# Performance work log

Measured on AMD Instinct MI355X. Metric: run time of the kernel, lower is better.

## Reference

```python
import jax, jax.numpy as jnp
import numpy as np

N_WAY = 5
K_SHOT = 5
TEMPERATURE = 1.0
NEG = -1e9  # emulates 'column does not exist' for pad columns beyond umask_length
EPS = 1e-12  # matches torch F.normalize eps


def _l2n(x, axis):
    n = jnp.sqrt(jnp.sum(x * x, axis=axis, keepdims=True))
    return x / jnp.maximum(n, EPS)


def setup_inputs() -> dict:
    key = jax.random.key(0)
    k1, k2, k3, k4, k5 = jax.random.split(key, 5)
    b, c, h, w = 4, 64, 5, 5
    q, u = 75, 100
    support_xf = jax.random.normal(k1, (b, N_WAY * K_SHOT, c, h, w), jnp.float32)
    query_xf = jax.random.normal(k2, (b, q, c, h, w), jnp.float32)
    unlabeled_xf = jax.random.normal(k3, (b, u, c, h, w), jnp.float32)
    support_y = jax.random.randint(k4, (b, N_WAY * K_SHOT), 0, N_WAY)
    query_y = jax.random.randint(k5, (b, q), 0, N_WAY)
    return {"support_xf": support_xf, "support_y": support_y, "query_xf": query_xf,
            "query_y": query_y, "unlabeled_xf": unlabeled_xf}


def _forward(support_xf, query_xf, unlabeled_xf, query_y):
    b, q, c, h, w = query_xf.shape
    M_s = K_SHOT * h * w
    unl = unlabeled_xf.reshape(b, -1, c, h, w)
    u = unl.shape[1]
    M_u = u * h * w
    # pooled unlabeled local descriptors, flattened in (u, h, w) order -> [b, c, M_u]
    unl_feat = unl.transpose(0, 2, 1, 3, 4).reshape(b, c, M_u)
    # support -> [b, n_way, c, k_shot*h*w]
    sup = support_xf.reshape(b, N_WAY, K_SHOT, c, h, w).transpose(0, 1, 3, 2, 4, 5).reshape(b, N_WAY, c, M_s)
    # cosine similarity unlabeled -> support: [b, n_way, M_u, M_s]
    u2s = jnp.einsum('bwcn,bcm->bwmn', _l2n(sup, 2), _l2n(unl_feat, 1))
    pool = u2s.transpose(0, 2, 1, 3).reshape(b, M_u, N_WAY * M_s)
    s_nearest = jnp.argmax(pool, axis=1)          # per support loc: nearest unlabeled loc
    u_nearest = jnp.argmax(pool, axis=2)          # per unlabeled loc: nearest support loc
    mutual = jnp.take_along_axis(s_nearest, u_nearest, axis=1) == jnp.arange(M_u)[None, :]  # [b, M_u]
    # class with max similarity per unlabeled location
    cls = jnp.argmax(jnp.max(u2s, axis=-1), axis=1)  # [b, M_u]
    umask = jax.nn.one_hot(cls, N_WAY, dtype=jnp.float32).transpose(0, 2, 1) \
            * mutual[:, None, :].astype(jnp.float32)  # [b, n_way, M_u]
    counts = umask.sum(-1)                          # [b, n_way]
    L = counts.max()                                # umask_length (traced)
    # stream compaction via stable argsort of the 0/1 mask (preserves original order)
    order = jnp.argsort(-umask, axis=-1)            # jnp.argsort is stable
    pts = unl_feat.transpose(0, 2, 1)               # [b, M_u, c]
    gath = jnp.take_along_axis(pts[:, None, :, :], order[..., None], axis=2)  # [b, n_way, M_u, c]
    valid = (jnp.arange(M_u)[None, None, :] < counts[:, :, None]).astype(jnp.float32)
    comp = gath * valid[..., None]                  # rows beyond count are zeros (as in torch)
    s_cat = jnp.concatenate([sup, comp.transpose(0, 1, 3, 2)], axis=-1)  # [b, n_way, c, M_s+M_u]
    M_tot = M_s + M_u
    qn = _l2n(query_xf.reshape(b, q, c, h * w), 2)
    scn = _l2n(s_cat, 2)
    sim = jnp.einsum('bqcm,bwcn->bqwmn', qn, scn)   # [b, q, n_way, M_q, M_tot]
    sim = (sim + 1.0) * 0.5                          # FourLayer_64F branch
    # columns beyond umask_length don't exist in the torch dense tensor -> exclude from maxes
    pad = jnp.arange(M_tot)[None, None, None, None, :] >= (M_s + L)
    sim = jnp.where(pad, NEG, sim)
    M_q = h * w
    qm = sim.transpose(0, 1, 3, 2, 4).reshape(b, q, M_q, N_WAY * M_tot)
    support_nearest = jnp.argmax(qm, axis=2)        # [b, q, n_way*M_tot]
    query_nearest = jnp.argmax(qm, axis=3)          # [b, q, M_q]
    g = jnp.take_along_axis(support_nearest, query_nearest, axis=2)
    q_mask = (g == jnp.arange(M_q)[None, None, :]).astype(sim.dtype)  # mutual NN mask
    query_value = (jnp.max(sim, axis=-1) * q_mask[:, :, None, :]).sum(-1)  # [b, q, n_way]
    logits = query_value.reshape(b * q, N_WAY) / TEMPERATURE
    y = query_y.reshape(b * q)
    logp = jax.nn.log_softmax(logits, axis=-1)
    loss = -jnp.take_along_axis(logp, y[:, None], axis=1).mean()
    return loss


def reference(support_xf, support_y, query_xf, query_y, unlabeled_xf):
    return _forward(support_xf, query_xf, unlabeled_xf, query_y)
```

## Files before the change

### kernel.cpp

```cpp
#include <hip/hip_runtime.h>

#define NEGINF (-1e30f)

constexpr size_t OF_UNL  = 0;
constexpr size_t OF_COLT = OF_UNL  + (size_t)4*2500*64;
constexpr size_t OF_QT   = OF_COLT + (size_t)20*64*256;
constexpr size_t OF_ROWV = OF_QT   + (size_t)300*64*25;
constexpr size_t OF_ROWI = OF_ROWV + (size_t)4*5*8*2500;
constexpr size_t OF_CVI  = OF_ROWI + (size_t)4*5*8*2500;
constexpr size_t OF_CMP  = OF_CVI  + (size_t)4*5*125*20*2;
constexpr size_t OF_CNT  = OF_CMP  + (size_t)4*5*2500;
constexpr size_t OF_UNEAR= OF_CNT  + 20;
constexpr size_t OF_SNEAR= OF_UNEAR+ 10000;
constexpr size_t OF_BV   = OF_SNEAR+ 2500;
constexpr size_t OF_BP   = OF_BV   + 37500;
constexpr size_t OF_AMX  = OF_BP   + 37500;

__global__ __launch_bounds__(256) void knorm(
    const float* __restrict__ sup, const float* __restrict__ qry,
    const float* __restrict__ unl,
    float* __restrict__ unl_n, float* __restrict__ colT,
    float* __restrict__ qt)
{
    int gid = blockIdx.x * 256 + threadIdx.x;
    int loc = gid >> 4;
    int sub = gid & 15;
    if (loc >= 20000) return;

    const float* src;
    float* dst1; int dstr1;

    if (loc < 10000) {
        int b = loc / 2500, m = loc % 2500;
        int u = m / 25, hw = m % 25;
        src  = unl + ((size_t)(b*100 + u) * 64) * 25 + hw;
        dst1 = unl_n + (size_t)loc * 64; dstr1 = 1;
    } else if (loc < 12500) {
        int idx = loc - 10000;
        int b = idx / 625, r = idx % 625;
        int w = r / 125,  n = r % 125;
        int shot = n / 25, hw = n % 25;
        src  = sup + ((size_t)(b*25 + w*5 + shot) * 64) * 25 + hw;
        dst1 = colT + ((size_t)(b*5 + w) * 64) * 256 + n; dstr1 = 256;
    } else {
        int idx = loc - 12500;
        int bq = idx / 25, mq = idx % 25;
        src  = qry + ((size_t)bq * 64) * 25 + mq;
        dst1 = qt + ((size_t)bq * 25 + mq) * 64; dstr1 = 1;
    }

    float v[4]; float ss = 0.f;
    int c0 = sub * 4;
#pragma unroll
    for (int j = 0; j < 4; ++j) { v[j] = src[(size_t)(c0 + j) * 25]; ss += v[j] * v[j]; }
#pragma unroll
    for (int msk = 1; msk < 16; msk <<= 1) ss += __shfl_xor(ss, msk);
    float sc = 1.f / fmaxf(sqrtf(ss), 1e-12f);
#pragma unroll
    for (int j = 0; j < 4; ++j)
        dst1[(size_t)(c0 + j) * dstr1] = v[j] * sc;
}

__global__ __launch_bounds__(256) void kb(
    const float* __restrict__ unl_n, const float* __restrict__ colT,
    float* __restrict__ rowv, int* __restrict__ rowi, float* __restrict__ colvi)
{
    int bid = blockIdx.x;
    int nc = bid & 3;
    int mb = (bid >> 2) % 20;
    int bw = bid / 80;
    int b  = bw / 5;
    int tid = threadIdx.x;
    int lane = tid & 63, wv = tid >> 6;

    __shared__ float uls[128 * 65];
    __shared__ float sls[64 * 36];
    __shared__ float sv_[4][32];
    __shared__ int   si_[4][32];

    int m0 = mb * 128;
    int n0 = nc * 32;

    for (int i = tid; i < 128 * 16; i += 256) {
        int row = i >> 4, c4 = (i & 15) * 4;
        int m = m0 + row;
        float4 x = make_float4(0.f, 0.f, 0.f, 0.f);
        if (m < 2500) x = *(const float4*)(unl_n + ((size_t)(b * 2500 + m)) * 64 + c4);
        uls[row * 65 + c4 + 0] = x.x;
        uls[row * 65 + c4 + 1] = x.y;
        uls[row * 65 + c4 + 2] = x.z;
        uls[row * 65 + c4 + 3] = x.w;
    }
    {
        int c = tid >> 2, q = tid & 3;
        const float* sp = colT + ((size_t)bw * 64 + c) * 256 + n0 + q * 8;
        float4 a = *(const float4*)sp;
        float4 d4 = *(const float4*)(sp + 4);
        float* d = &sls[c * 36 + q * 8];
        d[0] = a.x; d[1] = a.y; d[2] = a.z; d[3] = a.w;
        d[4] = d4.x; d[5] = d4.y; d[6] = d4.z; d[7] = d4.w;
    }
    __syncthreads();

    int ml = tid & 127;
    int m  = m0 + ml;
    int nh = tid >> 7;
    int nbase = nh * 16;
    int nn_total = (125 - n0) < 32 ? (125 - n0) : 32;
    const float* myrow = &uls[ml * 65];

    float acc[16];
#pragma unroll
    for (int j = 0; j < 16; ++j) acc[j] = 0.f;

    for (int c = 0; c < 64; ++c) {
        float uv = myrow[c];
        const float4* sr = (const float4*)&sls[c * 36 + nbase];
        float4 s0 = sr[0], s1 = sr[1], s2 = sr[2], s3 = sr[3];
        acc[0]  = fmaf(uv, s0.x, acc[0]);  acc[1]  = fmaf(uv, s0.y, acc[1]);
        acc[2]  = fmaf(uv, s0.z, acc[2]);  acc[3]  = fmaf(uv, s0.w, acc[3]);
        acc[4]  = fmaf(uv, s1.x, acc[4]);  acc[5]  = fmaf(uv, s1.y, acc[5]);
        acc[6]  = fmaf(uv, s1.z, acc[6]);  acc[7]  = fmaf(uv, s1.w, acc[7]);
        acc[8]  = fmaf(uv, s2.x, acc[8]);  acc[9]  = fmaf(uv, s2.y, acc[9]);
        acc[10] = fmaf(uv, s2.z, acc[10]); acc[11] = fmaf(uv, s2.w, acc[11]);
        acc[12] = fmaf(uv, s3.x, acc[12]); acc[13] = fmaf(uv, s3.y, acc[13]);
        acc[14] = fmaf(uv, s3.z, acc[14]); acc[15] = fmaf(uv, s3.w, acc[15]);
    }

    int nnloc = nn_total - nbase;
    nnloc = nnloc < 0 ? 0 : (nnloc > 16 ? 16 : nnloc);
    float rbv = NEGINF; int rbi = 0;
    for (int j = 0; j < nnloc; ++j)
        if (acc[j] > rbv) { rbv = acc[j]; rbi = n0 + nbase + j; }
    if (m < 2500) {
        int ck = nc * 2 + nh;
        rowv[((size_t)bw * 8 + ck) * 2500 + m] = rbv;
        rowi[((size_t)bw * 8 + ck) * 2500 + m] = rbi;
    }

#pragma unroll
    for (int j = 0; j < 16; ++j) {
        float v = (m < 2500 && (nbase + j) < nn_total) ? acc[j] : NEGINF;
        float vm = v;
#pragma unroll
        for (int s2 = 1; s2 < 64; s2 <<= 1) vm = fmaxf(vm, __shfl_xor(vm, s2));
        unsigned long long msk = __ballot(v == vm);
        int first = __ffsll((unsigned long long)msk) - 1;
        if (lane == 0) { sv_[wv][nbase + j] = vm; si_[wv][nbase + j] = m0 + (wv & 1) * 64 + first; }
    }
    __syncthreads();
    if (tid < nn_total) {
        int w0 = (tid < 16) ? 0 : 2;
        float v = sv_[w0][tid];     int vi = si_[w0][tid];
        float v2 = sv_[w0 + 1][tid]; int i2 = si_[w0 + 1][tid];
        if (v2 > v || (v2 == v && i2 < vi)) { v = v2; vi = i2; }
        float* cv = colvi + ((((size_t)bw) * 125 + (n0 + tid)) * 20 + mb) * 2;
        cv[0] = v; ((int*)cv)[1] = vi;
    }
}

__global__ __launch_bounds__(256) void kmerge(
    const float* __restrict__ rowv, const int* __restrict__ rowi,
    const float* __restrict__ colvi,
    int* __restrict__ unear, int* __restrict__ snear)
{
    int it = blockIdx.x * 256 + threadIdx.x;
    if (it < 10000) {
        int b = it / 2500, m = it % 2500;
        float bv = NEGINF; int bi = 0;
#pragma unroll
        for (int w = 0; w < 5; ++w) {
#pragma unroll
            for (int ck = 0; ck < 8; ++ck) {
                size_t o = (((size_t)(b * 5 + w)) * 8 + ck) * 2500 + m;
                float v = rowv[o];
                if (v > bv) { bv = v; bi = w * 125 + rowi[o]; }
            }
        }
        unear[it] = bi;
    } else if (it < 12500) {
        int idx = it - 10000;
        const float* p = colvi + (size_t)idx * 40;
        float bv = NEGINF; int bi = 0x7fffffff;
        for (int mb2 = 0; mb2 < 20; ++mb2) {
            float v = p[mb2 * 2]; int vi = ((const int*)p)[mb2 * 2 + 1];
            if (v > bv || (v == bv && vi < bi)) { bv = v; bi = vi; }
        }
        snear[idx] = bi;
    }
}

__global__ __launch_bounds__(256) void kcmp(
    const int* __restrict__ unear, const int* __restrict__ snear,
    const float* __restrict__ unl_n,
    int* __restrict__ cmp, int* __restrict__ cntg, float* __restrict__ colT)
{
    int p = blockIdx.x;
    int b = p / 5, way = p % 5;
    int tid = threadIdx.x, lane = tid & 63, wv = tid >> 6;
    __shared__ unsigned long long masks[40];
    __shared__ int base[40];
    __shared__ int tot_s;

    for (int ch = wv; ch < 40; ch += 4) {
        int m = ch * 64 + lane;
        bool ok = false;
        if (m < 2500) {
            int un = unear[b * 2500 + m];
            ok = (un / 125 == way) && (snear[b * 625 + un] == m);
        }
        unsigned long long msk = __ballot(ok ? 1 : 0);
        if (lane == 0) masks[ch] = msk;
    }
    __syncthreads();
    if (tid == 0) {
        int s = 0;
        for (int ch = 0; ch < 40; ++ch) { base[ch] = s; s += __popcll(masks[ch]); }
        cntg[p] = s; tot_s = s;
    }
    __syncthreads();
    for (int ch = wv; ch < 40; ch += 4) {
        unsigned long long msk = masks[ch];
        if ((msk >> lane) & 1ull) {
            int pre = __popcll(msk & ((1ull << lane) - 1ull));
            cmp[(size_t)p * 2500 + base[ch] + pre] = ch * 64 + lane;
        }
    }
    __syncthreads();
    int tot = tot_s;
    for (int t = tid; t < tot * 64; t += 256) {
        int i = t >> 6, c = t & 63;
        int m = cmp[(size_t)p * 2500 + i];
        colT[((size_t)p * 64 + c) * 256 + 125 + i] =
            unl_n[((size_t)(b * 2500 + m)) * 64 + c];
    }
}

__global__ __launch_bounds__(320) void kc1(
    const float* __restrict__ qt, const float* __restrict__ colT,
    const int* __restrict__ cntg,
    float* __restrict__ bvg, int* __restrict__ bpg,
    unsigned char* __restrict__ amaxg)
{
    int bid = blockIdx.x;
    int w = bid % 5, bq = bid / 5;
    int b = bq / 75;
    int bw = b * 5 + w;
    int tid = threadIdx.x;
    int lane = tid & 63, ty = tid >> 6;

    int L = 0;
#pragma unroll
    for (int i = 0; i < 20; ++i) { int v = cntg[i]; L = L > v ? L : v; }
    int cntw = 0, wb = 0;
#pragma unroll
    for (int w2 = 0; w2 < 5; ++w2) {
        int c2 = cntg[b * 5 + w2];
        if (w2 < w) wb += 125 + c2;
        if (w2 == w) cntw = c2;
    }
    int cw = 125 + cntw;

    __shared__ float qls[1600];
    __shared__ float amv[5][256];
    __shared__ unsigned char ami[5][256];
    __shared__ float redv[5][5];
    __shared__ int   redp[5][5];

    for (int i = tid; i < 1600; i += 320) qls[i] = qt[(size_t)bq * 1600 + i];
    __syncthreads();

    const float* cbase = colT + ((size_t)bw * 64) * 256 + lane * 4;
    float acc[5][4];
#pragma unroll
    for (int i = 0; i < 5; ++i)
#pragma unroll
        for (int j = 0; j < 4; ++j) acc[i][j] = 0.f;

    for (int c4 = 0; c4 < 16; ++c4) {
        float4 cv0 = *(const float4*)(cbase + (size_t)(c4 * 4 + 0) * 256);
        float4 cv1 = *(const float4*)(cbase + (size_t)(c4 * 4 + 1) * 256);
        float4 cv2 = *(const float4*)(cbase + (size_t)(c4 * 4 + 2) * 256);
        float4 cv3 = *(const float4*)(cbase + (size_t)(c4 * 4 + 3) * 256);
#pragma unroll
        for (int i = 0; i < 5; ++i) {
            float4 qv = *(const float4*)&qls[(ty * 5 + i) * 64 + c4 * 4];
            acc[i][0] = fmaf(cv0.x, qv.x, fmaf(cv1.x, qv.y, fmaf(cv2.x, qv.z, fmaf(cv3.x, qv.w, acc[i][0]))));
            acc[i][1] = fmaf(cv0.y, qv.x, fmaf(cv1.y, qv.y, fmaf(cv2.y, qv.z, fmaf(cv3.y, qv.w, acc[i][1]))));
            acc[i][2] = fmaf(cv0.z, qv.x, fmaf(cv1.z, qv.y, fmaf(cv2.z, qv.z, fmaf(cv3.z, qv.w, acc[i][2]))));
            acc[i][3] = fmaf(cv0.w, qv.x, fmaf(cv1.w, qv.y, fmaf(cv2.w, qv.z, fmaf(cv3.w, qv.w, acc[i][3]))));
        }
    }

    float cmax[4]; int cam[4];
#pragma unroll
    for (int j = 0; j < 4; ++j) { cmax[j] = NEGINF; cam[j] = 0; }
#pragma unroll
    for (int i = 0; i < 5; ++i)
#pragma unroll
        for (int j = 0; j < 4; ++j) {
            float s = (acc[i][j] + 1.0f) * 0.5f;
            acc[i][j] = s;
            if (s > cmax[j]) { cmax[j] = s; cam[j] = ty * 5 + i; }
        }
    *(float4*)&amv[ty][lane * 4] = make_float4(cmax[0], cmax[1], cmax[2], cmax[3]);
    {
        unsigned int pk = (unsigned)cam[0] | ((unsigned)cam[1] << 8) |
                          ((unsigned)cam[2] << 16) | ((unsigned)cam[3] << 24);
        ((unsigned int*)&ami[ty][0])[lane] = pk;
    }

#pragma unroll
    for (int i = 0; i < 5; ++i) {
        float bv = NEGINF; int bp = 0x7fffffff;
#pragma unroll
        for (int j = 0; j < 4; ++j) {
            int n = lane * 4 + j;
            if (n < cw) {
                float s = acc[i][j];
                if (s > bv) { bv = s; bp = ((w * 2625 + n) << 12) | (wb + n); }
            }
        }
        float vm = bv;
#pragma unroll
        for (int s2 = 1; s2 < 64; s2 <<= 1) vm = fmaxf(vm, __shfl_xor(vm, s2));
        int p = (bv == vm) ? bp : 0x7fffffff;
#pragma unroll
        for (int s2 = 1; s2 < 64; s2 <<= 1) p = min(p, __shfl_xor(p, s2));
        if (lane == 0) { redv[ty][i] = vm; redp[ty][i] = p; }
    }
    __syncthreads();

    if (tid < 256) {
        int col = tid;
        if (col < cw) {
            float v = amv[0][col]; int g = ami[0][col];
#pragma unroll
            for (int t2 = 1; t2 < 5; ++t2)
                if (amv[t2][col] > v) { v = amv[t2][col]; g = ami[t2][col]; }
            amaxg[(size_t)bq * 3200 + (wb + col)] = (unsigned char)g;
        }
    }
    if (tid < 25) {
        int t2 = tid / 5, i = tid % 5;
        float v = redv[t2][i]; int p = redp[t2][i];
        if (L > cntw) {
            int pp = ((w * 2625 + 125 + cntw) << 12) | 0xFFF;
            if (0.5f > v || (0.5f == v && pp < p)) { v = 0.5f; p = pp; }
        }
        size_t o = ((size_t)bq * 5 + w) * 25 + tid;
        bvg[o] = v; bpg[o] = p;
    }
}

__global__ __launch_bounds__(64) void kce(
    const float* __restrict__ bvg, const int* __restrict__ bpg,
    const unsigned char* __restrict__ amaxg, const int* __restrict__ qy,
    float* __restrict__ out)
{
    int bq = blockIdx.x;
    int tid = threadIdx.x;
    __shared__ float qmask[25];
    __shared__ float lg[5];
    if (tid < 25) {
        float v = NEGINF; int p = 0x7fffffff;
#pragma unroll
        for (int w = 0; w < 5; ++w) {
            size_t o = ((size_t)bq * 5 + w) * 25 + tid;
            float v2 = bvg[o]; int p2 = bpg[o];
            if (v2 > v || (v2 == v && p2 < p)) { v = v2; p = p2; }
        }
        int pos = p & 0xFFF;
        int g = (pos == 0xFFF) ? 0 : (int)amaxg[(size_t)bq * 3200 + pos];
        qmask[tid] = (g == tid) ? 1.0f : 0.0f;
    }
    __syncthreads();
    if (tid < 5) {
        float s = 0.f;
#pragma unroll
        for (int mq = 0; mq < 25; ++mq)
            s += bvg[((size_t)bq * 5 + tid) * 25 + mq] * qmask[mq];
        lg[tid] = s;
    }
    __syncthreads();
    if (tid == 0) {
        int y = qy[bq];
        float mx = lg[0];
#pragma unroll
        for (int w = 1; w < 5; ++w) mx = fmaxf(mx, lg[w]);
        float se = 0.f;
#pragma unroll
        for (int w = 0; w < 5; ++w) se += expf(lg[w] - mx);
        float loss = -(lg[y] - mx - logf(se));
        atomicAdd(out, loss * (1.0f / 300.0f));
    }
}

extern "C" void kernel_launch(void* const* d_in, const int* in_sizes, int n_in,
                              void* d_out, int out_size, void* d_ws, size_t ws_size,
                              hipStream_t stream)
{
    const float* sup = (const float*)d_in[0];
    const float* qry = (const float*)d_in[2];
    const int*   qy  = (const int*)d_in[3];
    const float* unl = (const float*)d_in[4];

    float* ws    = (float*)d_ws;
    float* unl_n = ws + OF_UNL;
    float* colT  = ws + OF_COLT;
    float* qt    = ws + OF_QT;
    float* rowv  = ws + OF_ROWV;
    int*   rowi  = (int*)(ws + OF_ROWI);
    float* colvi = ws + OF_CVI;
    int*   cmp   = (int*)(ws + OF_CMP);
    int*   cntg  = (int*)(ws + OF_CNT);
    int*   unear = (int*)(ws + OF_UNEAR);
    int*   snear = (int*)(ws + OF_SNEAR);
    float* bvg   = ws + OF_BV;
    int*   bpg   = (int*)(ws + OF_BP);
    unsigned char* amaxg = (unsigned char*)(ws + OF_AMX);

    hipMemsetAsync(d_out, 0, sizeof(float), stream);

    hipLaunchKernelGGL(knorm, dim3(1250), dim3(256), 0, stream,
                       sup, qry, unl, unl_n, colT, qt);
    hipLaunchKernelGGL(kb, dim3(1600), dim3(256), 0, stream,
                       unl_n, colT, rowv, rowi, colvi);
    hipLaunchKernelGGL(kmerge, dim3(49), dim3(256), 0, stream,
                       rowv, rowi, colvi, unear, snear);
    hipLaunchKernelGGL(kcmp, dim3(20), dim3(256), 0, stream,
                       unear, snear, unl_n, cmp, cntg, colT);
    hipLaunchKernelGGL(kc1, dim3(1500), dim3(320), 0, stream,
                       qt, colT, cntg, bvg, bpg, amaxg);
    hipLaunchKernelGGL(kce, dim3(300), dim3(64), 0, stream,
                       bvg, bpg, amaxg, qy, (float*)d_out);
}
```

Before: 183.0 us.

## Stage normalization through shared memory and double per-thread rows in similarity kernel

The normalization kernel now gives one block to each 64x25 feature map. The block loads the map contiguously into shared memory, computes the 25 norms there, and writes transposed normalized outputs, which replaces the strided 25-element global reads. The similarity kernel now handles 256 unlabeled rows per block with two accumulator sets per thread, so it reuses each support value from shared memory twice and halves the number of blocks and column partials. The cost is higher register and LDS pressure, which may reduce occupancy, and the norm step only uses 25 threads serially.

Result: slower. 193.0 us (+5.5%).

```diff
diff --git a/kernel.cpp b/kernel.cpp
--- a/kernel.cpp
+++ b/kernel.cpp
@@ -8,7 +8,7 @@
 constexpr size_t OF_ROWV = OF_QT   + (size_t)300*64*25;
 constexpr size_t OF_ROWI = OF_ROWV + (size_t)4*5*8*2500;
 constexpr size_t OF_CVI  = OF_ROWI + (size_t)4*5*8*2500;
-constexpr size_t OF_CMP  = OF_CVI  + (size_t)4*5*125*20*2;
+constexpr size_t OF_CMP  = OF_CVI  + (size_t)4*5*125*10*2;
 constexpr size_t OF_CNT  = OF_CMP  + (size_t)4*5*2500;
 constexpr size_t OF_UNEAR= OF_CNT  + 20;
 constexpr size_t OF_SNEAR= OF_UNEAR+ 10000;
@@ -22,43 +22,48 @@
     float* __restrict__ unl_n, float* __restrict__ colT,
     float* __restrict__ qt)
 {
-    int gid = blockIdx.x * 256 + threadIdx.x;
-    int loc = gid >> 4;
-    int sub = gid & 15;
-    if (loc >= 20000) return;
+    int u_id = blockIdx.x;
+    int tid = threadIdx.x;
+    __shared__ float ls[1600];
+    __shared__ float sc[25];
 
     const float* src;
-    float* dst1; int dstr1;
-
-    if (loc < 10000) {
-        int b = loc / 2500, m = loc % 2500;
-        int u = m / 25, hw = m % 25;
-        src  = unl + ((size_t)(b*100 + u) * 64) * 25 + hw;
-        dst1 = unl_n + (size_t)loc * 64; dstr1 = 1;
-    } else if (loc < 12500) {
-        int idx = loc - 10000;
-        int b = idx / 625, r = idx % 625;
-        int w = r / 125,  n = r % 125;
-        int shot = n / 25, hw = n % 25;
-        src  = sup + ((size_t)(b*25 + w*5 + shot) * 64) * 25 + hw;
-        dst1 = colT + ((size_t)(b*5 + w) * 64) * 256 + n; dstr1 = 256;
+    if (u_id < 400)      src = unl + (size_t)u_id * 1600;
+    else if (u_id < 500) src = sup + (size_t)(u_id - 400) * 1600;
+    else                 src = qry + (size_t)(u_id - 500) * 1600;
+
+    for (int i = tid; i < 1600; i += 256) ls[i] = src[i];
+    __syncthreads();
+    if (tid < 25) {
+        float ss = 0.f;
+        for (int c = 0; c < 64; ++c) { float v = ls[c * 25 + tid]; ss += v * v; }
+        sc[tid] = 1.f / fmaxf(sqrtf(ss), 1e-12f);
+    }
+    __syncthreads();
+
+    if (u_id < 400) {
+        int b = u_id / 100, u = u_id % 100;
+        float* dst = unl_n + ((size_t)b * 2500 + u * 25) * 64;
+        for (int i = tid; i < 1600; i += 256) {
+            int hw = i >> 6, c = i & 63;
+            dst[hw * 64 + c] = ls[c * 25 + hw] * sc[hw];
+        }
+    } else if (u_id < 500) {
+        int s = u_id - 400;
+        int b = s / 25, r = s % 25, w = r / 5, shot = r % 5;
+        float* dst = colT + ((size_t)(b * 5 + w) * 64) * 256 + shot * 25;
+        for (int i = tid; i < 1600; i += 256) {
+            int c = i / 25, hw = i % 25;
+            dst[c * 256 + hw] = ls[c * 25 + hw] * sc[hw];
+        }
     } else {
-        int idx = loc - 12500;
-        int bq = idx / 25, mq = idx % 25;
-        src  = qry + ((size_t)bq * 64) * 25 + mq;
-        dst1 = qt + ((size_t)bq * 25 + mq) * 64; dstr1 = 1;
-    }
-
-    float v[4]; float ss = 0.f;
-    int c0 = sub * 4;
-#pragma unroll
-    for (int j = 0; j < 4; ++j) { v[j] = src[(size_t)(c0 + j) * 25]; ss += v[j] * v[j]; }
-#pragma unroll
-    for (int msk = 1; msk < 16; msk <<= 1) ss += __shfl_xor(ss, msk);
-    float sc = 1.f / fmaxf(sqrtf(ss), 1e-12f);
-#pragma unroll
-    for (int j = 0; j < 4; ++j)
-        dst1[(size_t)(c0 + j) * dstr1] = v[j] * sc;
+        int bq = u_id - 500;
+        float* dst = qt + (size_t)bq * 1600;
+        for (int i = tid; i < 1600; i += 256) {
+            int hw = i >> 6, c = i & 63;
+            dst[hw * 64 + c] = ls[c * 25 + hw] * sc[hw];
+        }
+    }
 }
 
 __global__ __launch_bounds__(256) void kb(
@@ -67,21 +72,21 @@
 {
     int bid = blockIdx.x;
     int nc = bid & 3;
-    int mb = (bid >> 2) % 20;
-    int bw = bid / 80;
+    int mb = (bid >> 2) % 10;
+    int bw = bid / 40;
     int b  = bw / 5;
     int tid = threadIdx.x;
     int lane = tid & 63, wv = tid >> 6;
 
-    __shared__ float uls[128 * 65];
+    __shared__ float uls[256 * 65];
     __shared__ float sls[64 * 36];
     __shared__ float sv_[4][32];
     __shared__ int   si_[4][32];
 
-    int m0 = mb * 128;
+    int m0 = mb * 256;
     int n0 = nc * 32;
 
-    for (int i = tid; i < 128 * 16; i += 256) {
+    for (int i = tid; i < 256 * 16; i += 256) {
         int row = i >> 4, c4 = (i & 15) * 4;
         int m = m0 + row;
         float4 x = make_float4(0.f, 0.f, 0.f, 0.f);
@@ -103,50 +108,72 @@
     __syncthreads();
 
     int ml = tid & 127;
-    int m  = m0 + ml;
     int nh = tid >> 7;
     int nbase = nh * 16;
     int nn_total = (125 - n0) < 32 ? (125 - n0) : 32;
-    const float* myrow = &uls[ml * 65];
-
-    float acc[16];
-#pragma unroll
-    for (int j = 0; j < 16; ++j) acc[j] = 0.f;
+    int m_a = m0 + ml, m_b = m0 + ml + 128;
+    const float* rowA = &uls[ml * 65];
+    const float* rowB = &uls[(ml + 128) * 65];
+
+    float acc_a[16], acc_b[16];
+#pragma unroll
+    for (int j = 0; j < 16; ++j) { acc_a[j] = 0.f; acc_b[j] = 0.f; }
 
     for (int c = 0; c < 64; ++c) {
-        float uv = myrow[c];
+        float ua = rowA[c], ub = rowB[c];
         const float4* sr = (const float4*)&sls[c * 36 + nbase];
         float4 s0 = sr[0], s1 = sr[1], s2 = sr[2], s3 = sr[3];
-        acc[0]  = fmaf(uv, s0.x, acc[0]);  acc[1]  = fmaf(uv, s0.y, acc[1]);
-        acc[2]  = fmaf(uv, s0.z, acc[2]);  acc[3]  = fmaf(uv, s0.w, acc[3]);
-        acc[4]  = fmaf(uv, s1.x, acc[4]);  acc[5]  = fmaf(uv, s1.y, acc[5]);
-        acc[6]  = fmaf(uv, s1.z, acc[6]);  acc[7]  = fmaf(uv, s1.w, acc[7]);
-        acc[8]  = fmaf(uv, s2.x, acc[8]);  acc[9]  = fmaf(uv, s2.y, acc[9]);
-        acc[10] = fmaf(uv, s2.z, acc[10]); acc[11] = fmaf(uv, s2.w, acc[11]);
-        acc[12] = fmaf(uv, s3.x, acc[12]); acc[13] = fmaf(uv, s3.y, acc[13]);
-        acc[14] = fmaf(uv, s3.z, acc[14]); acc[15] = fmaf(uv, s3.w, acc[15]);
+        acc_a[0]  = fmaf(ua, s0.x, acc_a[0]);  acc_b[0]  = fmaf(ub, s0.x, acc_b[0]);
+        acc_a[1]  = fmaf(ua, s0.y, acc_a[1]);  acc_b[1]  = fmaf(ub, s0.y, acc_b[1]);
+        acc_a[2]  = fmaf(ua, s0.z, acc_a[2]);  acc_b[2]  = fmaf(ub, s0.z, acc_b[2]);
+        acc_a[3]  = fmaf(ua, s0.w, acc_a[3]);  acc_b[3]  = fmaf(ub, s0.w, acc_b[3]);
+        acc_a[4]  = fmaf(ua, s1.x, acc_a[4]);  acc_b[4]  = fmaf(ub, s1.x, acc_b[4]);
+        acc_a[5]  = fmaf(ua, s1.y, acc_a[5]);  acc_b[5]  = fmaf(ub, s1.y, acc_b[5]);
+        acc_a[6]  = fmaf(ua, s1.z, acc_a[6]);  acc_b[6]  = fmaf(ub, s1.z, acc_b[6]);
+        acc_a[7]  = fmaf(ua, s1.w, acc_a[7]);  acc_b[7]  = fmaf(ub, s1.w, acc_b[7]);
+        acc_a[8]  = fmaf(ua, s2.x, acc_a[8]);  acc_b[8]  = fmaf(ub, s2.x, acc_b[8]);
+        acc_a[9]  = fmaf(ua, s2.y, acc_a[9]);  acc_b[9]  = fmaf(ub, s2.y, acc_b[9]);
+        acc_a[10] = fmaf(ua, s2.z, acc_a[10]); acc_b[10] = fmaf(ub, s2.z, acc_b[10]);
+        acc_a[11] = fmaf(ua, s2.w, acc_a[11]); acc_b[11] = fmaf(ub, s2.w, acc_b[11]);
+        acc_a[12] = fmaf(ua, s3.x, acc_a[12]); acc_b[12] = fmaf(ub, s3.x, acc_b[12]);
+        acc_a[13] = fmaf(ua, s3.y, acc_a[13]); acc_b[13] = fmaf(ub, s3.y, acc_b[13]);
+        acc_a[14] = fmaf(ua, s3.z, acc_a[14]); acc_b[14] = fmaf(ub, s3.z, acc_b[14]);
+        acc_a[15] = fmaf(ua, s3.w, acc_a[15]); acc_b[15] = fmaf(ub, s3.w, acc_b[15]);
     }
 
     int nnloc = nn_total - nbase;
     nnloc = nnloc < 0 ? 0 : (nnloc > 16 ? 16 : nnloc);
-    float rbv = NEGINF; int rbi = 0;
-    for (int j = 0; j < nnloc; ++j)
-        if (acc[j] > rbv) { rbv = acc[j]; rbi = n0 + nbase + j; }
-    if (m < 2500) {
-        int ck = nc * 2 + nh;
-        rowv[((size_t)bw * 8 + ck) * 2500 + m] = rbv;
-        rowi[((size_t)bw * 8 + ck) * 2500 + m] = rbi;
+    int ck = nc * 2 + nh;
+    {
+        float rv = NEGINF; int ri = 0;
+        for (int j = 0; j < nnloc; ++j)
+            if (acc_a[j] > rv) { rv = acc_a[j]; ri = n0 + nbase + j; }
+        if (m_a < 2500) {
+            rowv[((size_t)bw * 8 + ck) * 2500 + m_a] = rv;
+            rowi[((size_t)bw * 8 + ck) * 2500 + m_a] = ri;
+        }
+        rv = NEGINF; ri = 0;
+        for (int j = 0; j < nnloc; ++j)
+            if (acc_b[j] > rv) { rv = acc_b[j]; ri = n0 + nbase + j; }
+        if (m_b < 2500) {
+            rowv[((size_t)bw * 8 + ck) * 2500 + m_b] = rv;
+            rowi[((size_t)bw * 8 + ck) * 2500 + m_b] = ri;
+        }
     }
 
 #pragma unroll
     for (int j = 0; j < 16; ++j) {
-        float v = (m < 2500 && (nbase + j) < nn_total) ? acc[j] : NEGINF;
-        float vm = v;
-#pragma unroll
-        for (int s2 = 1; s2 < 64; s2 <<= 1) vm = fmaxf(vm, __shfl_xor(vm, s2));
-        unsigned long long msk = __ballot(v == vm);
-        int first = __ffsll((unsigned long long)msk) - 1;
-        if (lane == 0) { sv_[wv][nbase + j] = vm; si_[wv][nbase + j] = m0 + (wv & 1) * 64 + first; }
+        bool jv = (nbase + j) < nn_total;
+        float va = (jv && m_a < 2500) ? acc_a[j] : NEGINF;
+        float vb = (jv && m_b < 2500) ? acc_b[j] : NEGINF;
+        float v; int vi;
+        if (vb > va) { v = vb; vi = m_b; } else { v = va; vi = m_a; }
+#pragma unroll
+        for (int s2 = 1; s2 < 64; s2 <<= 1) {
+            float v2 = __shfl_xor(v, s2); int i2 = __shfl_xor(vi, s2);
+            if (v2 > v || (v2 == v && i2 < vi)) { v = v2; vi = i2; }
+        }
+        if (lane == 0) { sv_[wv][nbase + j] = v; si_[wv][nbase + j] = vi; }
     }
     __syncthreads();
     if (tid < nn_total) {
@@ -154,7 +181,7 @@
         float v = sv_[w0][tid];     int vi = si_[w0][tid];
         float v2 = sv_[w0 + 1][tid]; int i2 = si_[w0 + 1][tid];
         if (v2 > v || (v2 == v && i2 < vi)) { v = v2; vi = i2; }
-        float* cv = colvi + ((((size_t)bw) * 125 + (n0 + tid)) * 20 + mb) * 2;
+        float* cv = colvi + ((((size_t)bw) * 125 + (n0 + tid)) * 10 + mb) * 2;
         cv[0] = v; ((int*)cv)[1] = vi;
     }
 }
@@ -180,9 +207,9 @@
         unear[it] = bi;
     } else if (it < 12500) {
         int idx = it - 10000;
-        const float* p = colvi + (size_t)idx * 40;
+        const float* p = colvi + (size_t)idx * 20;
         float bv = NEGINF; int bi = 0x7fffffff;
-        for (int mb2 = 0; mb2 < 20; ++mb2) {
+        for (int mb2 = 0; mb2 < 10; ++mb2) {
             float v = p[mb2 * 2]; int vi = ((const int*)p)[mb2 * 2 + 1];
             if (v > bv || (v == bv && vi < bi)) { bv = v; bi = vi; }
         }
@@ -422,9 +449,9 @@
 
     hipMemsetAsync(d_out, 0, sizeof(float), stream);
 
-    hipLaunchKernelGGL(knorm, dim3(1250), dim3(256), 0, stream,
+    hipLaunchKernelGGL(knorm, dim3(800), dim3(256), 0, stream,
                        sup, qry, unl, unl_n, colT, qt);
-    hipLaunchKernelGGL(kb, dim3(1600), dim3(256), 0, stream,
+    hipLaunchKernelGGL(kb, dim3(800), dim3(256), 0, stream,
                        unl_n, colT, rowv, rowi, colvi);
     hipLaunchKernelGGL(kmerge, dim3(49), dim3(256), 0, stream,
                        rowv, rowi, colvi, unear, snear);
```
